# Optimization experiments

Measured on AMD Instinct MI355X. Metric: run time of the kernel, lower is better.

Reference implementation:

```python
import jax, jax.numpy as jnp
import numpy as np

B, C, L, K = 8, 128, 32768, 129  # batch, seq_len (channels), samples, filter length


def setup_inputs() -> dict:
    key = jax.random.key(0)
    k0, k1, k2, k3 = jax.random.split(key, 4)
    return {
        "x": jax.random.normal(k0, (B, C, L), dtype=jnp.float32),
        "weights_mag": jnp.ones((C, 1), dtype=jnp.float32),
        "weights_angle": jax.random.uniform(k1, (C, 1), dtype=jnp.float32),
        "kernel_real": jax.random.normal(k2, (K,), dtype=jnp.float32),
        "kernel_imag": jax.random.normal(k3, (K,), dtype=jnp.float32),
    }


def _matched_filter(x, kr, ki):
    # PyTorch F.conv1d is cross-correlation; mf_coeffs = conj(kernel) repeated per
    # channel (groups = C), so every channel is correlated with the SAME conj kernel.
    # Input is real (x.to(complex64) has zero imag), so:
    #   out = corr(x, conj(k)) = corr(x, kr) - 1j * corr(x, ki)
    b, c, l = x.shape
    kk = kr.shape[0]
    pad = kk // 2
    w = jnp.stack([kr, -ki])[:, None, :]  # [2, 1, K]: real and imag of conj kernel
    y = jax.lax.conv_general_dilated(
        x.reshape(b * c, 1, l), w,
        window_strides=(1,), padding=[(pad, pad)],
        dimension_numbers=("NCH", "OIH", "NCH"),
    )  # [B*C, 2, L]
    yr = y[:, 0].reshape(b, c, l)
    yi = y[:, 1].reshape(b, c, l)
    return yr + 1j * yi  # complex64


def reference(x, weights_mag, weights_angle, kernel_real, kernel_imag):
    batch = x.shape[0]
    y = _matched_filter(x, kernel_real, kernel_imag)          # [B, C, L] complex64
    phase = jnp.arctan(weights_angle)                          # [C, 1]
    norm_mag = batch * jax.nn.softmax(weights_mag, axis=0)     # [C, 1]
    scale = (norm_mag.astype(jnp.complex64) * jnp.exp(-1j * phase))  # [C, 1] complex
    return scale * y
```

## Files before the change

kernel.cpp:

```cpp
#include <hip/hip_runtime.h>
#include <hip/hip_bf16.h>
#include <math.h>

constexpr int Bc = 8, Cc = 128, Lc = 32768, Kc = 129;

constexpr int MLEN = 256;
constexpr int T    = 8;
constexpr int NSEG = Lc / (MLEN * T);
constexpr int WPB  = 4;
constexpr int THREADS = 64 * WPB;
constexpr int LASTCW  = Lc / MLEN - 1;

typedef __attribute__((ext_vector_type(8))) short short8;
typedef __attribute__((ext_vector_type(4))) float floatx4;

#define WAITVM(N) do { asm volatile("s_waitcnt vmcnt(" #N ")" ::: "memory"); \
                       __builtin_amdgcn_sched_barrier(0); } while (0)

__device__ __forceinline__ unsigned short f2bf(float f) {
    return __builtin_bit_cast(unsigned short, __float2bfloat16(f));
}

__device__ __forceinline__ short8 cvt8(const float4& a, const float4& b) {
    __hip_bfloat162 p0 = __float22bfloat162_rn(make_float2(a.x, a.y));
    __hip_bfloat162 p1 = __float22bfloat162_rn(make_float2(a.z, a.w));
    __hip_bfloat162 p2 = __float22bfloat162_rn(make_float2(b.x, b.y));
    __hip_bfloat162 p3 = __float22bfloat162_rn(make_float2(b.z, b.w));
    ushort2 u0, u1, u2, u3;
    __builtin_memcpy(&u0, &p0, 4);
    __builtin_memcpy(&u1, &p1, 4);
    __builtin_memcpy(&u2, &p2, 4);
    __builtin_memcpy(&u3, &p3, 4);
    short8 r;
    r[0] = (short)u0.x; r[1] = (short)u0.y;
    r[2] = (short)u1.x; r[3] = (short)u1.y;
    r[4] = (short)u2.x; r[5] = (short)u2.y;
    r[6] = (short)u3.x; r[7] = (short)u3.y;
    return r;
}

__global__ void scale_kernel(const float* __restrict__ wm,
                             const float* __restrict__ wa,
                             float* __restrict__ ws, int C, float batchf) {
    int c = threadIdx.x;
    if (c >= C) return;
    float m = -1e30f;
    for (int i = 0; i < C; ++i) m = fmaxf(m, wm[i]);
    float s = 0.f;
    for (int i = 0; i < C; ++i) s += expf(wm[i] - m);
    float nm = batchf * expf(wm[c] - m) / s;
    float a = wa[c];
    float inv = rsqrtf(1.f + a * a);
    ws[2 * c]     = nm * inv;
    ws[2 * c + 1] = nm * a * inv;
}

__global__ __launch_bounds__(THREADS, 4)
void mf_kernel(const float* __restrict__ x,
               const float* __restrict__ kr,
               const float* __restrict__ ki,
               const float* __restrict__ sc_ss,
               float* __restrict__ out, int interleaved) {
    __shared__ __align__(16) unsigned short lb[WPB][2][512];

    const int seg = blockIdx.x;
    const int rg  = blockIdx.y;
    const int tid = threadIdx.x;
    const int lane= tid & 63;
    const int wv  = tid >> 6;
    const int fh  = lane >> 4;
    const int fn  = lane & 15;

    const int row = rg * WPB + wv;
    const int cw0 = seg * T;

    short8 br[5], bi[5];
    #pragma unroll
    for (int d = 0; d < 5; ++d) {
        #pragma unroll
        for (int e = 0; e < 8; ++e) {
            int idx = 32 * d + 8 * fh + e - fn;
            bool ok = (idx >= 0) && (idx < Kc);
            br[d][e] = (short)f2bf(ok ? kr[idx] : 0.f);
            bi[d][e] = (short)f2bf(ok ? ki[idx] : 0.f);
        }
    }

    const int ch = row & (Cc - 1);
    const float scv = sc_ss[2 * ch];
    const float ssv = sc_ss[2 * ch + 1];

    const float* __restrict__ xrow = x + (size_t)row * Lc;

    float4 F[2];
    auto ISSUE = [&](int cw) {
        int g = cw * MLEN - 64 + 8 * lane;
        g = min(max(g, 0), Lc - 8);
        F[0] = *reinterpret_cast<const float4*>(xrow + g);
        F[1] = *reinterpret_cast<const float4*>(xrow + g + 4);
    };

    ISSUE(cw0);
    WAITVM(0);
    {
        short8 h = cvt8(F[0], F[1]);
        *reinterpret_cast<short8*>(&lb[wv][0][8 * lane]) = h;
    }
    ISSUE(cw0 + 1);

    #pragma unroll
    for (int c = 0; c < T; ++c) {
        const int cw = cw0 + c;
        const int wb = c & 1;

        if (c + 1 < T) {
            if (c == 0) WAITVM(0);
            else        WAITVM(4);
            short8 h = cvt8(F[0], F[1]);
            *reinterpret_cast<short8*>(&lb[wv][wb ^ 1][8 * lane]) = h;
            if (c + 2 < T) ISSUE(cw + 2);
        }

        floatx4 cr = {0.f, 0.f, 0.f, 0.f};
        floatx4 ci = {0.f, 0.f, 0.f, 0.f};
        #pragma unroll
        for (int d = 0; d < 5; ++d) {
            short8 a = *reinterpret_cast<const short8*>(
                &lb[wv][wb][16 * fn + 8 * fh + 32 * d]);
            if (cw == 0) {
                if (2 * fn + fh + 4 * d < 8) a = short8{0,0,0,0,0,0,0,0};
            } else if (cw == LASTCW) {
                if (2 * fn + fh + 4 * d >= 40) a = short8{0,0,0,0,0,0,0,0};
            }
            cr = __builtin_amdgcn_mfma_f32_16x16x32_bf16(a, br[d], cr, 0, 0, 0);
            ci = __builtin_amdgcn_mfma_f32_16x16x32_bf16(a, bi[d], ci, 0, 0, 0);
        }

        if (!interleaved) {
            float* op = out + (size_t)row * Lc + cw * MLEN + 64 * fh + fn;
            #pragma unroll
            for (int r = 0; r < 4; ++r)
                op[16 * r] = scv * cr[r] - ssv * ci[r];
        } else {
            float2* op = reinterpret_cast<float2*>(out) +
                         ((size_t)row * Lc + cw * MLEN + 64 * fh + fn);
            #pragma unroll
            for (int r = 0; r < 4; ++r)
                op[16 * r] = make_float2(scv * cr[r] - ssv * ci[r],
                                         -scv * ci[r] - ssv * cr[r]);
        }
    }
}

extern "C" void kernel_launch(void* const* d_in, const int* in_sizes, int n_in,
                              void* d_out, int out_size, void* d_ws, size_t ws_size,
                              hipStream_t stream) {
    const float* x  = (const float*)d_in[0];
    const float* wm = (const float*)d_in[1];
    const float* wa = (const float*)d_in[2];
    const float* kr = (const float*)d_in[3];
    const float* ki = (const float*)d_in[4];
    float* out = (float*)d_out;
    float* ws  = (float*)d_ws;

    const int C = in_sizes[1];
    const long long N = (long long)Bc * Cc * Lc;
    const int interleaved = (out_size == 2 * N) ? 1 : 0;

    hipLaunchKernelGGL(scale_kernel, dim3(1), dim3(C), 0, stream,
                       wm, wa, ws, C, (float)Bc);

    dim3 grid(NSEG, (Bc * Cc) / WPB);
    hipLaunchKernelGGL(mf_kernel, grid, dim3(THREADS), 0, stream,
                       x, kr, ki, ws, out, interleaved);
}
```

Measured before the change: 81.01 us.

## Process two MFMA windows per iteration using a circular LDS ring buffer

Replaces the double-buffered 256-sample LDS windows with a 1024-entry per-wave circular ring. Each iteration now computes two 256-sample output chunks (512 samples) with four independent MFMA accumulator chains, and loads all LDS fragments before the next global chunk is staged. Segments per block double, halving the grid. This amortises waits and halo loads and raises MFMA ILP, at the cost of more registers and fewer blocks for latency hiding.

Measured after the change: 105.4 us. 30.2% more time.

```diff
diff --git a/kernel.cpp b/kernel.cpp
--- a/kernel.cpp
+++ b/kernel.cpp
@@ -4,12 +4,11 @@
 
 constexpr int Bc = 8, Cc = 128, Lc = 32768, Kc = 129;
 
-constexpr int MLEN = 256;
-constexpr int T    = 8;
-constexpr int NSEG = Lc / (MLEN * T);
-constexpr int WPB  = 4;
+constexpr int T     = 16;
+constexpr int NITER = T / 2;
+constexpr int NSEG  = Lc / (256 * T);
+constexpr int WPB   = 4;
 constexpr int THREADS = 64 * WPB;
-constexpr int LASTCW  = Lc / MLEN - 1;
 
 typedef __attribute__((ext_vector_type(8))) short short8;
 typedef __attribute__((ext_vector_type(4))) float floatx4;
@@ -61,7 +60,7 @@
                const float* __restrict__ ki,
                const float* __restrict__ sc_ss,
                float* __restrict__ out, int interleaved) {
-    __shared__ __align__(16) unsigned short lb[WPB][2][512];
+    __shared__ __align__(16) unsigned short lb[WPB][1024];
 
     const int seg = blockIdx.x;
     const int rg  = blockIdx.y;
@@ -70,9 +69,10 @@
     const int wv  = tid >> 6;
     const int fh  = lane >> 4;
     const int fn  = lane & 15;
+    const int v   = 2 * fn + fh;
 
     const int row = rg * WPB + wv;
-    const int cw0 = seg * T;
+    const int I0  = seg * NITER;
 
     short8 br[5], bi[5];
     #pragma unroll
@@ -91,63 +91,91 @@
     const float ssv = sc_ss[2 * ch + 1];
 
     const float* __restrict__ xrow = x + (size_t)row * Lc;
-
-    float4 F[2];
-    auto ISSUE = [&](int cw) {
-        int g = cw * MLEN - 64 + 8 * lane;
+    unsigned short* ring = &lb[wv][0];
+
+    float4 F0, F1;
+    auto ISSUE = [&](int Iw) {
+        int g = 512 * Iw + 960 + 8 * lane;
         g = min(max(g, 0), Lc - 8);
-        F[0] = *reinterpret_cast<const float4*>(xrow + g);
-        F[1] = *reinterpret_cast<const float4*>(xrow + g + 4);
+        F0 = *reinterpret_cast<const float4*>(xrow + g);
+        F1 = *reinterpret_cast<const float4*>(xrow + g + 4);
     };
 
-    ISSUE(cw0);
-    WAITVM(0);
     {
-        short8 h = cvt8(F[0], F[1]);
-        *reinterpret_cast<short8*>(&lb[wv][0][8 * lane]) = h;
+        int gA = 512 * I0 - 64 + 8 * lane;
+        int gB = 512 * I0 + 448 + 8 * lane;
+        gA = min(max(gA, 0), Lc - 8);
+        gB = min(max(gB, 0), Lc - 8);
+        float4 a0 = *reinterpret_cast<const float4*>(xrow + gA);
+        float4 a1 = *reinterpret_cast<const float4*>(xrow + gA + 4);
+        float4 b0 = *reinterpret_cast<const float4*>(xrow + gB);
+        float4 b1 = *reinterpret_cast<const float4*>(xrow + gB + 4);
+        WAITVM(0);
+        short8 ha = cvt8(a0, a1);
+        short8 hb = cvt8(b0, b1);
+        *reinterpret_cast<short8*>(&ring[8 * ((64 * I0 - 8 + lane) & 127)]) = ha;
+        *reinterpret_cast<short8*>(&ring[8 * ((64 * I0 + 56 + lane) & 127)]) = hb;
+        ISSUE(I0);
     }
-    ISSUE(cw0 + 1);
 
     #pragma unroll
-    for (int c = 0; c < T; ++c) {
-        const int cw = cw0 + c;
-        const int wb = c & 1;
-
-        if (c + 1 < T) {
-            if (c == 0) WAITVM(0);
-            else        WAITVM(4);
-            short8 h = cvt8(F[0], F[1]);
-            *reinterpret_cast<short8*>(&lb[wv][wb ^ 1][8 * lane]) = h;
-            if (c + 2 < T) ISSUE(cw + 2);
-        }
-
-        floatx4 cr = {0.f, 0.f, 0.f, 0.f};
-        floatx4 ci = {0.f, 0.f, 0.f, 0.f};
+    for (int i = 0; i < NITER; ++i) {
+        const int I = I0 + i;
+
+        short8 a0[5], a1[5];
         #pragma unroll
         for (int d = 0; d < 5; ++d) {
-            short8 a = *reinterpret_cast<const short8*>(
-                &lb[wv][wb][16 * fn + 8 * fh + 32 * d]);
-            if (cw == 0) {
-                if (2 * fn + fh + 4 * d < 8) a = short8{0,0,0,0,0,0,0,0};
-            } else if (cw == LASTCW) {
-                if (2 * fn + fh + 4 * d >= 40) a = short8{0,0,0,0,0,0,0,0};
+            const int s0 = (64 * I - 8 + v + 4 * d) & 127;
+            const int s1 = (64 * I + 24 + v + 4 * d) & 127;
+            a0[d] = *reinterpret_cast<const short8*>(&ring[8 * s0]);
+            a1[d] = *reinterpret_cast<const short8*>(&ring[8 * s1]);
+        }
+        if (I == 0) {
+            #pragma unroll
+            for (int d = 0; d < 5; ++d)
+                if (v + 4 * d < 8) a0[d] = short8{0,0,0,0,0,0,0,0};
+        }
+        if (I == 63) {
+            #pragma unroll
+            for (int d = 0; d < 5; ++d)
+                if (v + 4 * d >= 40) a1[d] = short8{0,0,0,0,0,0,0,0};
+        }
+        __builtin_amdgcn_sched_barrier(0);
+
+        if (i < NITER - 1) {
+            if (i == 0) WAITVM(0); else WAITVM(8);
+            short8 h = cvt8(F0, F1);
+            *reinterpret_cast<short8*>(&ring[8 * ((64 * I + 120 + lane) & 127)]) = h;
+            if (i < NITER - 2) ISSUE(I + 1);
+        }
+
+        floatx4 c0r = {0.f,0.f,0.f,0.f}, c0i = {0.f,0.f,0.f,0.f};
+        floatx4 c1r = {0.f,0.f,0.f,0.f}, c1i = {0.f,0.f,0.f,0.f};
+        #pragma unroll
+        for (int d = 0; d < 5; ++d) {
+            c0r = __builtin_amdgcn_mfma_f32_16x16x32_bf16(a0[d], br[d], c0r, 0, 0, 0);
+            c0i = __builtin_amdgcn_mfma_f32_16x16x32_bf16(a0[d], bi[d], c0i, 0, 0, 0);
+            c1r = __builtin_amdgcn_mfma_f32_16x16x32_bf16(a1[d], br[d], c1r, 0, 0, 0);
+            c1i = __builtin_amdgcn_mfma_f32_16x16x32_bf16(a1[d], bi[d], c1i, 0, 0, 0);
+        }
+
+        if (!interleaved) {
+            float* op = out + (size_t)row * Lc + 512 * I + 64 * fh + fn;
+            #pragma unroll
+            for (int r = 0; r < 4; ++r) {
+                op[16 * r]       = scv * c0r[r] - ssv * c0i[r];
+                op[16 * r + 256] = scv * c1r[r] - ssv * c1i[r];
             }
-            cr = __builtin_amdgcn_mfma_f32_16x16x32_bf16(a, br[d], cr, 0, 0, 0);
-            ci = __builtin_amdgcn_mfma_f32_16x16x32_bf16(a, bi[d], ci, 0, 0, 0);
-        }
-
-        if (!interleaved) {
-            float* op = out + (size_t)row * Lc + cw * MLEN + 64 * fh + fn;
-            #pragma unroll
-            for (int r = 0; r < 4; ++r)
-                op[16 * r] = scv * cr[r] - ssv * ci[r];
         } else {
             float2* op = reinterpret_cast<float2*>(out) +
-                         ((size_t)row * Lc + cw * MLEN + 64 * fh + fn);
-            #pragma unroll
-            for (int r = 0; r < 4; ++r)
-                op[16 * r] = make_float2(scv * cr[r] - ssv * ci[r],
-                                         -scv * ci[r] - ssv * cr[r]);
+                         ((size_t)row * Lc + 512 * I + 64 * fh + fn);
+            #pragma unroll
+            for (int r = 0; r < 4; ++r) {
+                op[16 * r]       = make_float2(scv * c0r[r] - ssv * c0i[r],
+                                               -scv * c0i[r] - ssv * c0r[r]);
+                op[16 * r + 256] = make_float2(scv * c1r[r] - ssv * c1i[r],
+                                               -scv * c1i[r] - ssv * c1r[r]);
+            }
         }
     }
 }
```
